# Performance work log

Hardware: AMD Instinct MI355X
Metric: run time of the kernel (lower is better)

The kernel has to match this reference:

```python
import jax, jax.numpy as jnp
import numpy as np

H = 896          # hidden_size
S = H // 2       # split_size = 448
Q = 256          # quantisation
B = 16384        # batch (parallel sampling streams)


def setup_inputs() -> dict:
    key = jax.random.key(0)
    ks = jax.random.split(key, 16)
    sc = 0.02
    return {
        "prev_y": jax.random.uniform(ks[0], (B, 2), dtype=jnp.float32),
        "prev_hidden": jax.random.normal(ks[1], (B, H), dtype=jnp.float32),
        "current_coarse": jax.random.uniform(ks[2], (B, 1), dtype=jnp.float32),
        # torch Linear weights are [out_features, in_features]
        "R_w": sc * jax.random.normal(ks[3], (3 * H, H), dtype=jnp.float32),
        "Ic_w": sc * jax.random.normal(ks[4], (3 * S, 2), dtype=jnp.float32),
        "If_w": sc * jax.random.normal(ks[5], (3 * S, 3), dtype=jnp.float32),
        "bias_u": jnp.zeros((H,), jnp.float32),
        "bias_r": jnp.zeros((H,), jnp.float32),
        "bias_e": jnp.zeros((H,), jnp.float32),
        "O1_w": sc * jax.random.normal(ks[6], (S, S), dtype=jnp.float32),
        "O1_b": jnp.zeros((S,), jnp.float32),
        "O2_w": sc * jax.random.normal(ks[7], (Q, S), dtype=jnp.float32),
        "O2_b": jnp.zeros((Q,), jnp.float32),
        "O3_w": sc * jax.random.normal(ks[8], (S, S), dtype=jnp.float32),
        "O3_b": jnp.zeros((S,), jnp.float32),
        "O4_w": sc * jax.random.normal(ks[9], (Q, S), dtype=jnp.float32),
        "O4_b": jnp.zeros((Q,), jnp.float32),
    }


def reference(prev_y, prev_hidden, current_coarse,
              R_w, Ic_w, If_w, bias_u, bias_r, bias_e,
              O1_w, O1_b, O2_w, O2_b, O3_w, O3_b, O4_w, O4_b):
    # recurrent projection: [B,H] @ [H,3H] -> [B,3H]
    R_hidden = prev_hidden @ R_w.T
    R_u, R_r, R_e = jnp.split(R_hidden, 3, axis=1)

    # coarse input projection: [B,2] -> [B,3S]
    cproj = prev_y @ Ic_w.T
    Ic_u, Ic_r, Ic_e = jnp.split(cproj, 3, axis=1)

    # fine input projection: [B,3] -> [B,3S]
    fine_in = jnp.concatenate([prev_y, current_coarse], axis=1)
    fproj = fine_in @ If_w.T
    If_u, If_r, If_e = jnp.split(fproj, 3, axis=1)

    I_u = jnp.concatenate([Ic_u, If_u], axis=1)  # [B,H]
    I_r = jnp.concatenate([Ic_r, If_r], axis=1)
    I_e = jnp.concatenate([Ic_e, If_e], axis=1)

    u = jax.nn.sigmoid(R_u + I_u + bias_u)
    r = jax.nn.sigmoid(R_r + I_r + bias_r)
    e = jnp.tanh(r * R_e + I_e + bias_e)
    hidden = u * prev_hidden + (1.0 - u) * e  # [B,H]

    h_coarse, h_fine = jnp.split(hidden, 2, axis=1)  # [B,S] each
    out_coarse = jax.nn.relu(h_coarse @ O1_w.T + O1_b) @ O2_w.T + O2_b  # [B,Q]
    out_fine = jax.nn.relu(h_fine @ O3_w.T + O3_b) @ O4_w.T + O4_b      # [B,Q]
    return (out_coarse, out_fine, hidden)
```

## Files before the change

kernel.cpp:

```cpp
#include <hip/hip_runtime.h>
#include <hip/hip_bf16.h>
#include <cstdint>

#define BB 16384
#define HH 896
#define SS 448
#define QQ 256
#define NPAD 2816

typedef __attribute__((ext_vector_type(4))) float f32x4;
typedef __attribute__((ext_vector_type(8))) short bf16x8;

__device__ __forceinline__ short f2bf(float f){
  union { float f; uint32_t u; } x; x.f = f;
  uint32_t r = (x.u + 0x7fffu + ((x.u >> 16) & 1u)) >> 16;
  return (short)r;
}
__device__ __forceinline__ float bf2f(short b){
  union { uint32_t u; float f; } x; x.u = ((uint32_t)(uint16_t)b) << 16;
  return x.f;
}

__global__ __launch_bounds__(256)
void castall_kernel(const float* __restrict__ ph, short* __restrict__ Ah,
                    const float* __restrict__ Rw, short* __restrict__ Rwh,
                    const float* __restrict__ O1w, short* __restrict__ O1b,
                    const float* __restrict__ O3w, short* __restrict__ O3b,
                    const float* __restrict__ O2w, short* __restrict__ O2b,
                    const float* __restrict__ O4w, short* __restrict__ O4b)
{
  int u = blockIdx.x * 256 + threadIdx.x;
  auto cp4 = [](short* d, const float* s, int jd, int js){
    float4 v = reinterpret_cast<const float4*>(s)[js];
    short4 o; o.x = f2bf(v.x); o.y = f2bf(v.y); o.z = f2bf(v.z); o.w = f2bf(v.w);
    reinterpret_cast<short4*>(d)[jd] = o;
  };
  auto z4 = [](short* d, int jd){
    short4 o; o.x = 0; o.y = 0; o.z = 0; o.w = 0;
    reinterpret_cast<short4*>(d)[jd] = o;
  };
  if (u < 3670016) { cp4(Ah, ph, u, u); return; }
  u -= 3670016;
  if (u < 602112) { cp4(Rwh, Rw, u, u); return; }
  u -= 602112;
  if (u < 28672) { z4(Rwh, 602112 + u); return; }
  u -= 28672;
  if (u < 57344) { if (u < 50176) cp4(O1b, O1w, u, u); else z4(O1b, u); return; }
  u -= 57344;
  if (u < 57344) { if (u < 50176) cp4(O3b, O3w, u, u); else z4(O3b, u); return; }
  u -= 57344;
  if (u < 32768) {
    int r = u >> 7, c4 = u & 127;
    if (c4 < 112) cp4(O2b, O2w, u, r * 112 + c4); else z4(O2b, u);
    return;
  }
  u -= 32768;
  if (u < 32768) {
    int r = u >> 7, c4 = u & 127;
    if (c4 < 112) cp4(O4b, O4w, u, r * 112 + c4); else z4(O4b, u);
    return;
  }
}

template<int EP>
__global__ __launch_bounds__(512, 2)
void gemm256_bt(const short* __restrict__ A0p, const short* __restrict__ A1p, int lda,
                const short* __restrict__ B0p, const short* __restrict__ B1p, int ldb,
                void* __restrict__ C0p, void* __restrict__ C1p, int ldc,
                const float* __restrict__ bias0, const float* __restrict__ bias1, int nbias,
                int Nvalid, int K, int nbn)
{
  const short* A  = blockIdx.z ? A1p : A0p;
  const short* Bt = blockIdx.z ? B1p : B0p;
  void* Cv        = blockIdx.z ? C1p : C0p;
  const float* bias = blockIdx.z ? bias1 : bias0;

  __shared__ short smem[65536];
  const int tid = threadIdx.x;
  const int w  = tid >> 6, ln = tid & 63;
  const int wr = w >> 2,  wc = w & 3;
  const int lr = ln & 15;
  const int lg = ln >> 4;
  const int srow = ln >> 3;
  const int sgc  = (ln & 7) ^ srow;

  int wg = blockIdx.x;
  const int cpx = gridDim.x >> 3;
  wg = (wg & 7) * cpx + (wg >> 3);
  const int bm = wg / nbn, bn = wg - bm * nbn;
  const long m0 = (long)bm * 256, n0 = (long)bn * 256;

  f32x4 acc[8][4] = {};

  auto stage = [&](const short* __restrict__ src, int ld, long rbase, int k0,
                   int lbase , int h) {
#pragma unroll
    for (int i = 0; i < 2; ++i) {
      const int rloc = h * 128 + i * 64 + w * 8;
      const short* g = src + (rbase + rloc + srow) * (long)ld + k0 + sgc * 8;
      __builtin_amdgcn_global_load_lds(
          (const __attribute__((address_space(1))) void*)g,
          (__attribute__((address_space(3))) void*)&smem[lbase + rloc * 64],
          16, 0, 0);
    }
  };
  auto rd = [&](int lbase, int r, int ks) -> bf16x8 {
    const int gc = ks * 4 + lg;
    return *reinterpret_cast<const bf16x8*>(&smem[lbase + r * 64 + ((gc ^ (r & 7)) << 3)]);
  };

  const int NT = K >> 6;
  stage(A,  lda, m0, 0, 0,     0);
  stage(Bt, ldb, n0, 0, 32768, 0);
  stage(Bt, ldb, n0, 0, 32768, 1);
  stage(A,  lda, m0, 0, 0,     1);
  asm volatile("s_waitcnt vmcnt(2)" ::: "memory");
  __builtin_amdgcn_s_barrier();
  asm volatile("" ::: "memory");

  for (int j = 0; j < NT; ++j) {
    const int Ab = (j & 1) * 16384;
    const int Bb = 32768 + (j & 1) * 16384;
    const int An = ((j + 1) & 1) * 16384;
    const int Bn = 32768 + ((j + 1) & 1) * 16384;
    const bool pf = (j + 1 < NT);
    const int k1 = (j + 1) << 6;
    bf16x8 b[4][2];

    __builtin_amdgcn_s_setprio(1);
    {
#pragma unroll
      for (int n = 0; n < 4; ++n)
#pragma unroll
        for (int ks = 0; ks < 2; ++ks)
          b[n][ks] = rd(Bb, wc * 64 + n * 16 + lr, ks);
      if (pf) {
        stage(A,  lda, m0, k1, An, 0);
        stage(Bt, ldb, n0, k1, Bn, 0);
        stage(Bt, ldb, n0, k1, Bn, 1);
        stage(A,  lda, m0, k1, An, 1);
      }
#pragma unroll
      for (int q = 0; q < 2; ++q) {
        bf16x8 a[2][2];
#pragma unroll
        for (int dm = 0; dm < 2; ++dm)
#pragma unroll
          for (int ks = 0; ks < 2; ++ks)
            a[dm][ks] = rd(Ab, q * 64 + dm * 32 + wr * 16 + lr, ks);
#pragma unroll
        for (int dm = 0; dm < 2; ++dm)
#pragma unroll
          for (int n = 0; n < 4; ++n)
#pragma unroll
            for (int ks = 0; ks < 2; ++ks)
              acc[2 * q + dm][n] = __builtin_amdgcn_mfma_f32_16x16x32_bf16(
                  a[dm][ks], b[n][ks], acc[2 * q + dm][n], 0, 0, 0);
      }
    }
    __builtin_amdgcn_s_setprio(0);
    if (pf) asm volatile("s_waitcnt vmcnt(8)" ::: "memory");
    else    asm volatile("s_waitcnt vmcnt(0)" ::: "memory");
    __builtin_amdgcn_s_barrier();
    asm volatile("" ::: "memory");

    __builtin_amdgcn_s_setprio(1);
    {
#pragma unroll
      for (int q = 2; q < 4; ++q) {
        bf16x8 a[2][2];
#pragma unroll
        for (int dm = 0; dm < 2; ++dm)
#pragma unroll
          for (int ks = 0; ks < 2; ++ks)
            a[dm][ks] = rd(Ab, q * 64 + dm * 32 + wr * 16 + lr, ks);
#pragma unroll
        for (int dm = 0; dm < 2; ++dm)
#pragma unroll
          for (int n = 0; n < 4; ++n)
#pragma unroll
            for (int ks = 0; ks < 2; ++ks)
              acc[2 * q + dm][n] = __builtin_amdgcn_mfma_f32_16x16x32_bf16(
                  a[dm][ks], b[n][ks], acc[2 * q + dm][n], 0, 0, 0);
      }
    }
    __builtin_amdgcn_s_setprio(0);
    asm volatile("s_waitcnt vmcnt(2)" ::: "memory");
    __builtin_amdgcn_s_barrier();
    asm volatile("" ::: "memory");
  }

  if (EP == 2) {
    const int lc = ln & 15, rg = lg * 4;
#pragma unroll
    for (int n = 0; n < 4; ++n) {
      const long col = n0 + wc * 64 + n * 16 + lc;
      const float bv = bias[col];
#pragma unroll
      for (int m = 0; m < 8; ++m) {
        const long row = m0 + m * 32 + wr * 16 + rg;
#pragma unroll
        for (int reg = 0; reg < 4; ++reg)
          ((float*)Cv)[(row + reg) * (long)ldc + col] = acc[m][n][reg] + bv;
      }
    }
    return;
  }

#pragma unroll
  for (int n = 0; n < 4; ++n) {
    const int col = wc * 64 + n * 16 + lr;
    const int gc = col >> 3, c7 = col & 7;
    float bv = 0.f;
    if (EP == 1) {
      const long gcol = n0 + col;
      bv = (gcol < nbias) ? bias[gcol] : 0.f;
    }
#pragma unroll
    for (int m = 0; m < 8; ++m) {
      const int row = m * 32 + wr * 16 + lg * 4;
#pragma unroll
      for (int reg = 0; reg < 4; ++reg) {
        float v = acc[m][n][reg];
        if (EP == 1) { v += bv; v = v > 0.f ? v : 0.f; }
        const int rr = row + reg;
        smem[rr * 256 + ((gc ^ ((rr >> 1) & 7)) << 3) + c7] = f2bf(v);
      }
    }
  }
  __builtin_amdgcn_s_barrier();
  const int rt = tid >> 5;
  const int ctg = (tid & 31);
  const long colg = n0 + ctg * 8;
  if (colg < Nvalid) {
#pragma unroll
    for (int p = 0; p < 16; ++p) {
      const int row = p * 16 + rt;
      bf16x8 v = *reinterpret_cast<const bf16x8*>(
          &smem[row * 256 + ((ctg ^ ((row >> 1) & 7)) << 3)]);
      *reinterpret_cast<bf16x8*>(&((short*)Cv)[(m0 + row) * (long)ldc + colg]) = v;
    }
  }
}

__global__ __launch_bounds__(256)
void gates_kernel(const float* __restrict__ prev_y,
                  const short* __restrict__ Ah,
                  const float* __restrict__ ccoarse,
                  const float* __restrict__ Icw,
                  const float* __restrict__ Ifw,
                  const float* __restrict__ bu,
                  const float* __restrict__ br,
                  const float* __restrict__ be,
                  const short* __restrict__ Rh,
                  float* __restrict__ hid_out,
                  short* __restrict__ hid_bf)
{
  const int v = blockIdx.x * 256 + threadIdx.x;
  const int b = v / 112;
  const int h0 = (v - b * 112) * 8;
  const long rbase = (long)b * (3 * HH);

  const bf16x8 ru8 = *reinterpret_cast<const bf16x8*>(Rh + rbase + h0);
  const bf16x8 rr8 = *reinterpret_cast<const bf16x8*>(Rh + rbase + HH + h0);
  const bf16x8 re8 = *reinterpret_cast<const bf16x8*>(Rh + rbase + 2 * HH + h0);
  const bf16x8 ah8 = *reinterpret_cast<const bf16x8*>(Ah + (long)b * HH + h0);
  const float py0 = prev_y[2 * b], py1 = prev_y[2 * b + 1], c0 = ccoarse[b];

  float iu[8], ir[8], ie[8];
  if (h0 < SS) {
    const float4* cu = reinterpret_cast<const float4*>(Icw + 2 * h0);
    const float4* cr = reinterpret_cast<const float4*>(Icw + 2 * (SS + h0));
    const float4* ce = reinterpret_cast<const float4*>(Icw + 2 * (2 * SS + h0));
#pragma unroll
    for (int q = 0; q < 4; ++q) {
      float4 a = cu[q]; iu[2*q] = py0*a.x + py1*a.y; iu[2*q+1] = py0*a.z + py1*a.w;
      float4 r = cr[q]; ir[2*q] = py0*r.x + py1*r.y; ir[2*q+1] = py0*r.z + py1*r.w;
      float4 e = ce[q]; ie[2*q] = py0*e.x + py1*e.y; ie[2*q+1] = py0*e.z + py1*e.w;
    }
  } else {
    const int j0 = h0 - SS;
    const float* fu = Ifw + 3 * j0;
    const float* fr = Ifw + 3 * (SS + j0);
    const float* fe = Ifw + 3 * (2 * SS + j0);
#pragma unroll
    for (int j = 0; j < 8; ++j) {
      iu[j] = py0 * fu[3*j] + py1 * fu[3*j+1] + c0 * fu[3*j+2];
      ir[j] = py0 * fr[3*j] + py1 * fr[3*j+1] + c0 * fr[3*j+2];
      ie[j] = py0 * fe[3*j] + py1 * fe[3*j+1] + c0 * fe[3*j+2];
    }
  }
  const float4* bu4 = reinterpret_cast<const float4*>(bu + h0);
  const float4* br4 = reinterpret_cast<const float4*>(br + h0);
  const float4* be4 = reinterpret_cast<const float4*>(be + h0);
  float buv[8], brv[8], bev[8];
  { float4 a = bu4[0], b2 = bu4[1];
    buv[0]=a.x; buv[1]=a.y; buv[2]=a.z; buv[3]=a.w; buv[4]=b2.x; buv[5]=b2.y; buv[6]=b2.z; buv[7]=b2.w; }
  { float4 a = br4[0], b2 = br4[1];
    brv[0]=a.x; brv[1]=a.y; brv[2]=a.z; brv[3]=a.w; brv[4]=b2.x; brv[5]=b2.y; brv[6]=b2.z; brv[7]=b2.w; }
  { float4 a = be4[0], b2 = be4[1];
    bev[0]=a.x; bev[1]=a.y; bev[2]=a.z; bev[3]=a.w; bev[4]=b2.x; bev[5]=b2.y; bev[6]=b2.z; bev[7]=b2.w; }

  float hd[8];
  bf16x8 hb;
#pragma unroll
  for (int j = 0; j < 8; ++j) {
    float u = 1.f / (1.f + __expf(-(bf2f(ru8[j]) + iu[j] + buv[j])));
    float r = 1.f / (1.f + __expf(-(bf2f(rr8[j]) + ir[j] + brv[j])));
    float e = tanhf(r * bf2f(re8[j]) + ie[j] + bev[j]);
    hd[j] = u * bf2f(ah8[j]) + (1.f - u) * e;
    hb[j] = f2bf(hd[j]);
  }
  float4* ho = reinterpret_cast<float4*>(hid_out + (long)b * HH + h0);
  ho[0] = make_float4(hd[0], hd[1], hd[2], hd[3]);
  ho[1] = make_float4(hd[4], hd[5], hd[6], hd[7]);
  *reinterpret_cast<bf16x8*>(hid_bf + (long)b * HH + h0) = hb;
}

extern "C" void kernel_launch(void* const* d_in, const int* in_sizes, int n_in,
                              void* d_out, int out_size, void* d_ws, size_t ws_size,
                              hipStream_t stream)
{
  (void)in_sizes; (void)n_in; (void)out_size; (void)ws_size;
  const float* prev_y      = (const float*)d_in[0];
  const float* prev_hidden = (const float*)d_in[1];
  const float* ccoarse     = (const float*)d_in[2];
  const float* R_w  = (const float*)d_in[3];
  const float* Ic_w = (const float*)d_in[4];
  const float* If_w = (const float*)d_in[5];
  const float* bu   = (const float*)d_in[6];
  const float* br   = (const float*)d_in[7];
  const float* be   = (const float*)d_in[8];
  const float* O1w  = (const float*)d_in[9];
  const float* O1b  = (const float*)d_in[10];
  const float* O2w  = (const float*)d_in[11];
  const float* O2b  = (const float*)d_in[12];
  const float* O3w  = (const float*)d_in[13];
  const float* O3b  = (const float*)d_in[14];
  const float* O4w  = (const float*)d_in[15];
  const float* O4b  = (const float*)d_in[16];

  float* out_coarse = (float*)d_out;
  float* out_fine   = out_coarse + (long)BB * QQ;
  float* hidden     = out_fine + (long)BB * QQ;

  char* ws = (char*)d_ws;
  short* Ah   = (short*)(ws + 0);
  short* Rwh  = (short*)(ws + 29360128);
  short* Rh   = (short*)(ws + 34406400);
  short* hidb = (short*)(ws + 122486784);
  short* O1wb = (short*)(ws + 151846912);
  short* O3wb = (short*)(ws + 152305664);
  short* O2wb = (short*)(ws + 152764416);
  short* O4wb = (short*)(ws + 153026560);
  short* t1   = (short*)(ws + 0);
  short* t2   = (short*)(ws + 16777216);

  castall_kernel<<<17504, 256, 0, stream>>>(prev_hidden, Ah, R_w, Rwh,
                                            O1w, O1wb, O3w, O3wb, O2w, O2wb, O4w, O4wb);

  gemm256_bt<0><<<dim3(704, 1, 1), 512, 0, stream>>>(
      Ah, Ah, HH, Rwh, Rwh, HH, Rh, Rh, 3 * HH,
      nullptr, nullptr, 0, 3 * HH, HH, NPAD / 256);

  gates_kernel<<<BB * 112 / 256, 256, 0, stream>>>(prev_y, Ah, ccoarse,
                                                   Ic_w, If_w, bu, br, be, Rh, hidden, hidb);

  gemm256_bt<1><<<dim3(128, 1, 2), 512, 0, stream>>>(
      hidb, hidb + 448, HH, O1wb, O3wb, 448, t1, t2, 512,
      O1b, O3b, 448, 512, 448, 2);

  gemm256_bt<2><<<dim3(64, 1, 2), 512, 0, stream>>>(
      t1, t2, 512, O2wb, O4wb, 512, out_coarse, out_fine, QQ,
      O2b, O4b, QQ, QQ, 512, 1);
}
```

Before: 215.4 us.

## Fuse GRU gate computation into recurrent GEMM via last-block-per-row atomic counter

Removes the separate gates kernel launch. Each block of the recurrent GEMM increments a per-row-tile counter after writing its output, and the last block to finish a row tile of 256 rows computes the gates and hidden state for that tile. The counters are zeroed in the cast kernel. This saves one launch and lets gate work overlap with GEMM tail blocks, but only 64 blocks do the gate work serially over 256x896 elements each, which may add a tail, and it adds fence and atomic overhead to every block.

Result: slower. 627.9 us (+191.6%).

```diff
diff --git a/kernel.cpp b/kernel.cpp
--- a/kernel.cpp
+++ b/kernel.cpp
@@ -27,7 +27,8 @@
                     const float* __restrict__ O1w, short* __restrict__ O1b,
                     const float* __restrict__ O3w, short* __restrict__ O3b,
                     const float* __restrict__ O2w, short* __restrict__ O2b,
-                    const float* __restrict__ O4w, short* __restrict__ O4b)
+                    const float* __restrict__ O4w, short* __restrict__ O4b,
+                    int* __restrict__ cnt)
 {
   int u = blockIdx.x * 256 + threadIdx.x;
   auto cp4 = [](short* d, const float* s, int jd, int js){
@@ -60,6 +61,10 @@
     if (c4 < 112) cp4(O4b, O4w, u, r * 112 + c4); else z4(O4b, u);
     return;
   }
+  u -= 32768;
+  if (u < 16) {
+    reinterpret_cast<int4*>(cnt)[u] = int4{0, 0, 0, 0};
+  }
 }
 
 template<int EP>
@@ -68,7 +73,13 @@
                 const short* __restrict__ B0p, const short* __restrict__ B1p, int ldb,
                 void* __restrict__ C0p, void* __restrict__ C1p, int ldc,
                 const float* __restrict__ bias0, const float* __restrict__ bias1, int nbias,
-                int Nvalid, int K, int nbn)
+                int Nvalid, int K, int nbn,
+                int* __restrict__ cnt,
+                const float* __restrict__ prev_y, const float* __restrict__ ccoarse,
+                const float* __restrict__ Icw, const float* __restrict__ Ifw,
+                const float* __restrict__ bu, const float* __restrict__ br,
+                const float* __restrict__ be,
+                float* __restrict__ hid_out, short* __restrict__ hid_bf)
 {
   const short* A  = blockIdx.z ? A1p : A0p;
   const short* Bt = blockIdx.z ? B1p : B0p;
@@ -76,6 +87,7 @@
   const float* bias = blockIdx.z ? bias1 : bias0;
 
   __shared__ short smem[65536];
+  __shared__ int lastf;
   const int tid = threadIdx.x;
   const int w  = tid >> 6, ln = tid & 63;
   const int wr = w >> 2,  wc = w & 3;
@@ -229,92 +241,95 @@
     }
   }
   __builtin_amdgcn_s_barrier();
-  const int rt = tid >> 5;
-  const int ctg = (tid & 31);
-  const long colg = n0 + ctg * 8;
-  if (colg < Nvalid) {
-#pragma unroll
-    for (int p = 0; p < 16; ++p) {
-      const int row = p * 16 + rt;
-      bf16x8 v = *reinterpret_cast<const bf16x8*>(
-          &smem[row * 256 + ((ctg ^ ((row >> 1) & 7)) << 3)]);
-      *reinterpret_cast<bf16x8*>(&((short*)Cv)[(m0 + row) * (long)ldc + colg]) = v;
-    }
-  }
-}
-
-__global__ __launch_bounds__(256)
-void gates_kernel(const float* __restrict__ prev_y,
-                  const short* __restrict__ Ah,
-                  const float* __restrict__ ccoarse,
-                  const float* __restrict__ Icw,
-                  const float* __restrict__ Ifw,
-                  const float* __restrict__ bu,
-                  const float* __restrict__ br,
-                  const float* __restrict__ be,
-                  const short* __restrict__ Rh,
-                  float* __restrict__ hid_out,
-                  short* __restrict__ hid_bf)
-{
-  const int v = blockIdx.x * 256 + threadIdx.x;
-  const int b = v / 112;
-  const int h0 = (v - b * 112) * 8;
-  const long rbase = (long)b * (3 * HH);
-
-  const bf16x8 ru8 = *reinterpret_cast<const bf16x8*>(Rh + rbase + h0);
-  const bf16x8 rr8 = *reinterpret_cast<const bf16x8*>(Rh + rbase + HH + h0);
-  const bf16x8 re8 = *reinterpret_cast<const bf16x8*>(Rh + rbase + 2 * HH + h0);
-  const bf16x8 ah8 = *reinterpret_cast<const bf16x8*>(Ah + (long)b * HH + h0);
-  const float py0 = prev_y[2 * b], py1 = prev_y[2 * b + 1], c0 = ccoarse[b];
-
-  float iu[8], ir[8], ie[8];
-  if (h0 < SS) {
-    const float4* cu = reinterpret_cast<const float4*>(Icw + 2 * h0);
-    const float4* cr = reinterpret_cast<const float4*>(Icw + 2 * (SS + h0));
-    const float4* ce = reinterpret_cast<const float4*>(Icw + 2 * (2 * SS + h0));
-#pragma unroll
-    for (int q = 0; q < 4; ++q) {
-      float4 a = cu[q]; iu[2*q] = py0*a.x + py1*a.y; iu[2*q+1] = py0*a.z + py1*a.w;
-      float4 r = cr[q]; ir[2*q] = py0*r.x + py1*r.y; ir[2*q+1] = py0*r.z + py1*r.w;
-      float4 e = ce[q]; ie[2*q] = py0*e.x + py1*e.y; ie[2*q+1] = py0*e.z + py1*e.w;
-    }
-  } else {
-    const int j0 = h0 - SS;
-    const float* fu = Ifw + 3 * j0;
-    const float* fr = Ifw + 3 * (SS + j0);
-    const float* fe = Ifw + 3 * (2 * SS + j0);
-#pragma unroll
-    for (int j = 0; j < 8; ++j) {
-      iu[j] = py0 * fu[3*j] + py1 * fu[3*j+1] + c0 * fu[3*j+2];
-      ir[j] = py0 * fr[3*j] + py1 * fr[3*j+1] + c0 * fr[3*j+2];
-      ie[j] = py0 * fe[3*j] + py1 * fe[3*j+1] + c0 * fe[3*j+2];
-    }
-  }
-  const float4* bu4 = reinterpret_cast<const float4*>(bu + h0);
-  const float4* br4 = reinterpret_cast<const float4*>(br + h0);
-  const float4* be4 = reinterpret_cast<const float4*>(be + h0);
-  float buv[8], brv[8], bev[8];
-  { float4 a = bu4[0], b2 = bu4[1];
-    buv[0]=a.x; buv[1]=a.y; buv[2]=a.z; buv[3]=a.w; buv[4]=b2.x; buv[5]=b2.y; buv[6]=b2.z; buv[7]=b2.w; }
-  { float4 a = br4[0], b2 = br4[1];
-    brv[0]=a.x; brv[1]=a.y; brv[2]=a.z; brv[3]=a.w; brv[4]=b2.x; brv[5]=b2.y; brv[6]=b2.z; brv[7]=b2.w; }
-  { float4 a = be4[0], b2 = be4[1];
-    bev[0]=a.x; bev[1]=a.y; bev[2]=a.z; bev[3]=a.w; bev[4]=b2.x; bev[5]=b2.y; bev[6]=b2.z; bev[7]=b2.w; }
-
-  float hd[8];
-  bf16x8 hb;
-#pragma unroll
-  for (int j = 0; j < 8; ++j) {
-    float u = 1.f / (1.f + __expf(-(bf2f(ru8[j]) + iu[j] + buv[j])));
-    float r = 1.f / (1.f + __expf(-(bf2f(rr8[j]) + ir[j] + brv[j])));
-    float e = tanhf(r * bf2f(re8[j]) + ie[j] + bev[j]);
-    hd[j] = u * bf2f(ah8[j]) + (1.f - u) * e;
-    hb[j] = f2bf(hd[j]);
-  }
-  float4* ho = reinterpret_cast<float4*>(hid_out + (long)b * HH + h0);
-  ho[0] = make_float4(hd[0], hd[1], hd[2], hd[3]);
-  ho[1] = make_float4(hd[4], hd[5], hd[6], hd[7]);
-  *reinterpret_cast<bf16x8*>(hid_bf + (long)b * HH + h0) = hb;
+  {
+    const int rt = tid >> 5;
+    const int ctg = (tid & 31);
+    const long colg = n0 + ctg * 8;
+    if (colg < Nvalid) {
+#pragma unroll
+      for (int p = 0; p < 16; ++p) {
+        const int row = p * 16 + rt;
+        bf16x8 v = *reinterpret_cast<const bf16x8*>(
+            &smem[row * 256 + ((ctg ^ ((row >> 1) & 7)) << 3)]);
+        *reinterpret_cast<bf16x8*>(&((short*)Cv)[(m0 + row) * (long)ldc + colg]) = v;
+      }
+    }
+  }
+
+  if (EP == 0) {
+    __threadfence();
+    if (tid == 0) {
+      int old = atomicAdd(cnt + bm, 1);
+      lastf = (old == nbn - 1);
+    }
+    __syncthreads();
+    if (!lastf) return;
+    __threadfence();
+
+    const short* Rh = (const short*)Cv;
+    const short* Ahp = A0p;
+    for (int ch = tid; ch < 256 * 112; ch += 512) {
+      const int rr = ch / 112, c8 = ch - rr * 112;
+      const int h0 = c8 * 8;
+      const long brow = m0 + rr;
+      const long rbase = brow * (3 * HH);
+
+      const bf16x8 ru8 = *reinterpret_cast<const bf16x8*>(Rh + rbase + h0);
+      const bf16x8 rr8 = *reinterpret_cast<const bf16x8*>(Rh + rbase + HH + h0);
+      const bf16x8 re8 = *reinterpret_cast<const bf16x8*>(Rh + rbase + 2 * HH + h0);
+      const bf16x8 ah8 = *reinterpret_cast<const bf16x8*>(Ahp + brow * HH + h0);
+      const float py0 = prev_y[2 * brow], py1 = prev_y[2 * brow + 1], c0 = ccoarse[brow];
+
+      float iu[8], ir[8], ie[8];
+      if (h0 < SS) {
+        const float4* cu = reinterpret_cast<const float4*>(Icw + 2 * h0);
+        const float4* cr = reinterpret_cast<const float4*>(Icw + 2 * (SS + h0));
+        const float4* ce = reinterpret_cast<const float4*>(Icw + 2 * (2 * SS + h0));
+#pragma unroll
+        for (int q = 0; q < 4; ++q) {
+          float4 a = cu[q]; iu[2*q] = py0*a.x + py1*a.y; iu[2*q+1] = py0*a.z + py1*a.w;
+          float4 r = cr[q]; ir[2*q] = py0*r.x + py1*r.y; ir[2*q+1] = py0*r.z + py1*r.w;
+          float4 e = ce[q]; ie[2*q] = py0*e.x + py1*e.y; ie[2*q+1] = py0*e.z + py1*e.w;
+        }
+      } else {
+        const int j0 = h0 - SS;
+        const float* fu = Ifw + 3 * j0;
+        const float* fr = Ifw + 3 * (SS + j0);
+        const float* fe = Ifw + 3 * (2 * SS + j0);
+#pragma unroll
+        for (int j = 0; j < 8; ++j) {
+          iu[j] = py0 * fu[3*j] + py1 * fu[3*j+1] + c0 * fu[3*j+2];
+          ir[j] = py0 * fr[3*j] + py1 * fr[3*j+1] + c0 * fr[3*j+2];
+          ie[j] = py0 * fe[3*j] + py1 * fe[3*j+1] + c0 * fe[3*j+2];
+        }
+      }
+      const float4* bu4 = reinterpret_cast<const float4*>(bu + h0);
+      const float4* br4 = reinterpret_cast<const float4*>(br + h0);
+      const float4* be4 = reinterpret_cast<const float4*>(be + h0);
+      float buv[8], brv[8], bev[8];
+      { float4 a = bu4[0], b2 = bu4[1];
+        buv[0]=a.x; buv[1]=a.y; buv[2]=a.z; buv[3]=a.w; buv[4]=b2.x; buv[5]=b2.y; buv[6]=b2.z; buv[7]=b2.w; }
+      { float4 a = br4[0], b2 = br4[1];
+        brv[0]=a.x; brv[1]=a.y; brv[2]=a.z; brv[3]=a.w; brv[4]=b2.x; brv[5]=b2.y; brv[6]=b2.z; brv[7]=b2.w; }
+      { float4 a = be4[0], b2 = be4[1];
+        bev[0]=a.x; bev[1]=a.y; bev[2]=a.z; bev[3]=a.w; bev[4]=b2.x; bev[5]=b2.y; bev[6]=b2.z; bev[7]=b2.w; }
+
+      float hd[8];
+      bf16x8 hb;
+#pragma unroll
+      for (int j = 0; j < 8; ++j) {
+        float u = 1.f / (1.f + __expf(-(bf2f(ru8[j]) + iu[j] + buv[j])));
+        float r = 1.f / (1.f + __expf(-(bf2f(rr8[j]) + ir[j] + brv[j])));
+        float e = tanhf(r * bf2f(re8[j]) + ie[j] + bev[j]);
+        hd[j] = u * bf2f(ah8[j]) + (1.f - u) * e;
+        hb[j] = f2bf(hd[j]);
+      }
+      float4* ho = reinterpret_cast<float4*>(hid_out + brow * HH + h0);
+      ho[0] = make_float4(hd[0], hd[1], hd[2], hd[3]);
+      ho[1] = make_float4(hd[4], hd[5], hd[6], hd[7]);
+      *reinterpret_cast<bf16x8*>(hid_bf + brow * HH + h0) = hb;
+    }
+  }
 }
 
 extern "C" void kernel_launch(void* const* d_in, const int* in_sizes, int n_in,
@@ -353,24 +368,28 @@
   short* O3wb = (short*)(ws + 152305664);
   short* O2wb = (short*)(ws + 152764416);
   short* O4wb = (short*)(ws + 153026560);
+  int*   cnt  = (int*)(ws + 153288704);
   short* t1   = (short*)(ws + 0);
   short* t2   = (short*)(ws + 16777216);
 
-  castall_kernel<<<17504, 256, 0, stream>>>(prev_hidden, Ah, R_w, Rwh,
-                                            O1w, O1wb, O3w, O3wb, O2w, O2wb, O4w, O4wb);
+  castall_kernel<<<17505, 256, 0, stream>>>(prev_hidden, Ah, R_w, Rwh,
+                                            O1w, O1wb, O3w, O3wb, O2w, O2wb, O4w, O4wb,
+                                            cnt);
 
   gemm256_bt<0><<<dim3(704, 1, 1), 512, 0, stream>>>(
       Ah, Ah, HH, Rwh, Rwh, HH, Rh, Rh, 3 * HH,
-      nullptr, nullptr, 0, 3 * HH, HH, NPAD / 256);
-
-  gates_kernel<<<BB * 112 / 256, 256, 0, stream>>>(prev_y, Ah, ccoarse,
-                                                   Ic_w, If_w, bu, br, be, Rh, hidden, hidb);
+      nullptr, nullptr, 0, 3 * HH, HH, 11,
+      cnt, prev_y, ccoarse, Ic_w, If_w, bu, br, be, hidden, hidb);
 
   gemm256_bt<1><<<dim3(128, 1, 2), 512, 0, stream>>>(
       hidb, hidb + 448, HH, O1wb, O3wb, 448, t1, t2, 512,
-      O1b, O3b, 448, 512, 448, 2);
+      O1b, O3b, 448, 512, 448, 2,
+      nullptr, nullptr, nullptr, nullptr, nullptr, nullptr, nullptr, nullptr,
+      nullptr, nullptr);
 
   gemm256_bt<2><<<dim3(64, 1, 2), 512, 0, stream>>>(
       t1, t2, 512, O2wb, O4wb, 512, out_coarse, out_fine, QQ,
-      O2b, O4b, QQ, QQ, 512, 1);
-}
+      O2b, O4b, QQ, QQ, 512, 1,
+      nullptr, nullptr, nullptr, nullptr, nullptr, nullptr, nullptr, nullptr,
+      nullptr, nullptr);
+}
```
